# Optimization experiments

Hardware: AMD Instinct MI355X
Metric: run time of the kernel (lower is better)

## Reference

```python
import jax, jax.numpy as jnp
import numpy as np

D_MODEL = 1024
N_STATE = 1024


def setup_inputs() -> dict:
    key = jax.random.key(0)
    k_x, k_A, k_Bw, k_Bb, k_Cw, k_Cb = jax.random.split(key, 6)
    x = jax.random.normal(k_x, (8, 2048, D_MODEL), dtype=jnp.float32)
    log_A = jax.random.normal(k_A, (N_STATE,), dtype=jnp.float32) * 0.1 - 1.0
    # nn.Linear default init: U(-1/sqrt(fan_in), 1/sqrt(fan_in)); weight is [out, in]
    bnd_B = 1.0 / np.sqrt(D_MODEL)
    B_w = jax.random.uniform(k_Bw, (N_STATE, D_MODEL), minval=-bnd_B, maxval=bnd_B, dtype=jnp.float32)
    B_b = jax.random.uniform(k_Bb, (N_STATE,), minval=-bnd_B, maxval=bnd_B, dtype=jnp.float32)
    bnd_C = 1.0 / np.sqrt(N_STATE)
    C_w = jax.random.uniform(k_Cw, (D_MODEL, N_STATE), minval=-bnd_C, maxval=bnd_C, dtype=jnp.float32)
    C_b = jax.random.uniform(k_Cb, (D_MODEL,), minval=-bnd_C, maxval=bnd_C, dtype=jnp.float32)
    return {"x": x, "log_A": log_A, "B_w": B_w, "B_b": B_b, "C_w": C_w, "C_b": C_b}


def _ssm_scan(A, B_x):
    """Diagonal linear recurrence h_t = A * h_{t-1} + B_x_t (h_0 prior = 0).

    Implemented as a parallel associative scan over the time axis.
    A: [N], B_x: [B, T, N] -> h: [B, T, N]
    """
    a = jnp.broadcast_to(A, B_x.shape)  # [B, T, N]

    def combine(c1, c2):
        a1, b1 = c1
        a2, b2 = c2
        return (a1 * a2, a2 * b1 + b2)

    _, h = jax.lax.associative_scan(combine, (a, B_x), axis=1)
    return h


def reference(x, log_A, B_w, B_b, C_w, C_b):
    A = jax.nn.sigmoid(log_A)                                  # [N]
    B_x = jnp.einsum('btd,nd->btn', x, B_w) + B_b              # [B, T, N]
    h = _ssm_scan(A, B_x)                                      # [B, T, N]
    y = jnp.einsum('btn,dn->btd', h, C_w) + C_b                # [B, T, D]
    return y
```

## Files before the change

### kernel.cpp

```cpp
#include <hip/hip_runtime.h>
#include <hip/hip_bf16.h>
#include <cstdint>
#include <cstddef>


typedef __attribute__((ext_vector_type(8))) short short8;
typedef __attribute__((ext_vector_type(4))) float f32x4;

#define AS_GLOBAL(p) ((const __attribute__((address_space(1))) void*)(p))
#define AS_LDS(p)    ((__attribute__((address_space(3))) void*)(p))

__device__ __forceinline__ unsigned short f2bf(float f) {
    union { float f; unsigned u; } v; v.f = f;
    return (unsigned short)((v.u + 0x7FFFu + ((v.u >> 16) & 1u)) >> 16);
}
__device__ __forceinline__ float bf2f(unsigned short u) {
    union { float f; unsigned u; } v; v.u = ((unsigned)u) << 16;
    return v.f;
}

__global__ void cvt_all(const float4* __restrict__ x, const float4* __restrict__ bw,
                        const float4* __restrict__ cw, ushort4* __restrict__ xo,
                        ushort4* __restrict__ bo, ushort4* __restrict__ co) {
    const int NX = (16384 * 1024) / 4;
    const int NW = (1024 * 1024) / 4;
    int i = blockIdx.x * blockDim.x + threadIdx.x;
    int stride = gridDim.x * blockDim.x;
    for (; i < NX + 2 * NW; i += stride) {
        const float4* s; ushort4* d; int j;
        if (i < NX)           { s = x;  d = xo; j = i; }
        else if (i < NX + NW) { s = bw; d = bo; j = i - NX; }
        else                  { s = cw; d = co; j = i - NX - NW; }
        float4 v = s[j];
        d[j] = make_ushort4(f2bf(v.x), f2bf(v.y), f2bf(v.z), f2bf(v.w));
    }
}

__global__ __launch_bounds__(256, 2)
void gemm1_scan_fused(const unsigned short* __restrict__ A,
                      const unsigned short* __restrict__ B,
                      const float* __restrict__ bias,
                      const float* __restrict__ logA,
                      unsigned short* __restrict__ H,
                      int M, int N, int K)
{
    constexpr int BK = 32, SXS = 130;
    __shared__ __align__(16) unsigned short smem[20800];
    unsigned short* As = smem;
    unsigned short* Bs = smem + 5120;
    unsigned short* Sx = smem;

    const int tid  = threadIdx.x;
    const int lane = tid & 63;
    const int wave = tid >> 6;
    const int wr   = wave >> 1;
    const int wm   = wr * 64;
    const int wn   = (wave & 1) * 64;
    const int q    = lane >> 4;
    const int l16  = lane & 15;
    const int m0   = blockIdx.x * 128;
    const int n0   = blockIdx.y * 128;

    const int rsub = lane >> 2;
    const int c8   = (lane & 3) * 8;

    f32x4 acc[4][4] = {};
    f32x4 accw[4]   = {};

    for (int k0 = 0; k0 < K; k0 += BK) {
        #pragma unroll
        for (int p = 0; p < 2; ++p) {
            const int rowbase = p * 64 + wave * 16;
            int gra = m0 - 32 + rowbase + rsub; if (gra < 0) gra = 0;
            const unsigned short* ga = A + (size_t)gra * K + k0 + c8;
            const unsigned short* gb = B + (size_t)(n0 + rowbase + rsub) * K + k0 + c8;
            __builtin_amdgcn_global_load_lds(AS_GLOBAL(ga), AS_LDS(&As[rowbase * BK]), 16, 0, 0);
            __builtin_amdgcn_global_load_lds(AS_GLOBAL(gb), AS_LDS(&Bs[rowbase * BK]), 16, 0, 0);
        }
        if (tid < 128) {
            const int rowbase = 128 + wave * 16;
            const unsigned short* ga = A + (size_t)(m0 - 32 + rowbase + rsub) * K + k0 + c8;
            __builtin_amdgcn_global_load_lds(AS_GLOBAL(ga), AS_LDS(&As[rowbase * BK]), 16, 0, 0);
        }
        __syncthreads();

        short8 a[4], aw, b[4];
        #pragma unroll
        for (int i = 0; i < 4; ++i)
            a[i] = *reinterpret_cast<const short8*>(&As[(32 + wm + i * 16 + l16) * BK + q * 8]);
        aw = *reinterpret_cast<const short8*>(&As[(wr * 16 + l16) * BK + q * 8]);
        #pragma unroll
        for (int j = 0; j < 4; ++j)
            b[j] = *reinterpret_cast<const short8*>(&Bs[(wn + j * 16 + l16) * BK + q * 8]);

        #pragma unroll
        for (int i = 0; i < 4; ++i)
            #pragma unroll
            for (int j = 0; j < 4; ++j)
                acc[i][j] = __builtin_amdgcn_mfma_f32_16x16x32_bf16(a[i], b[j], acc[i][j], 0, 0, 0);
        #pragma unroll
        for (int j = 0; j < 4; ++j)
            accw[j] = __builtin_amdgcn_mfma_f32_16x16x32_bf16(aw, b[j], accw[j], 0, 0, 0);
        __syncthreads();
    }

    float bcol[4];
    #pragma unroll
    for (int j = 0; j < 4; ++j)
        bcol[j] = bias[n0 + wn + j * 16 + l16];

    #pragma unroll
    for (int j = 0; j < 4; ++j) {
        #pragma unroll
        for (int r = 0; r < 4; ++r)
            Sx[(wr * 16 + q * 4 + r) * SXS + wn + j * 16 + l16] = f2bf(accw[j][r] + bcol[j]);
        #pragma unroll
        for (int i = 0; i < 4; ++i)
            #pragma unroll
            for (int r = 0; r < 4; ++r)
                Sx[(32 + wm + i * 16 + q * 4 + r) * SXS + wn + j * 16 + l16] = f2bf(acc[i][j][r] + bcol[j]);
    }
    __syncthreads();

    const int col  = tid & 127;
    const int half = tid >> 7;
    const int n    = n0 + col;
    const float Aa = 1.0f / (1.0f + __expf(-logA[n]));
    const bool chunk0 = (blockIdx.x & 15) == 0;

    float h = 0.0f;
    const int rw = half ? 64 : 0;
    if (!(half == 0 && chunk0)) {
        #pragma unroll
        for (int r = 0; r < 32; ++r)
            h = fmaf(Aa, h, bf2f(Sx[(rw + r) * SXS + col]));
    }
    const int rs = half ? 96 : 32;
    size_t o = (size_t)(m0 + (half ? 64 : 0)) * 1024 + n;
    #pragma unroll 8
    for (int r = 0; r < 64; ++r) {
        h = fmaf(Aa, h, bf2f(Sx[(rs + r) * SXS + col]));
        H[o] = f2bf(h);
        o += 1024;
    }
}

__global__ __launch_bounds__(256, 2)
void gemm_bf16_nt(const unsigned short* __restrict__ A,
                  const unsigned short* __restrict__ B,
                  const float* __restrict__ bias,
                  float* __restrict__ C,
                  int M, int N, int K)
{
    constexpr int BM = 128, BN = 128, BK = 32;
    __shared__ __align__(16) unsigned short As[BM * BK];
    __shared__ __align__(16) unsigned short Bs[BN * BK];

    const int tid  = threadIdx.x;
    const int lane = tid & 63;
    const int wave = tid >> 6;
    const int wm   = (wave >> 1) * 64;
    const int wn   = (wave & 1)  * 64;
    const int q    = lane >> 4;
    const int l16  = lane & 15;
    const int m0 = blockIdx.x * BM;
    const int n0 = blockIdx.y * BN;

    const int rsub = lane >> 2;
    const int c8   = (lane & 3) * 8;

    f32x4 acc[4][4] = {};

    for (int k0 = 0; k0 < K; k0 += BK) {
        #pragma unroll
        for (int p = 0; p < 2; ++p) {
            const int rowbase = p * 64 + wave * 16;
            const unsigned short* ga = A + (size_t)(m0 + rowbase + rsub) * K + k0 + c8;
            const unsigned short* gb = B + (size_t)(n0 + rowbase + rsub) * K + k0 + c8;
            __builtin_amdgcn_global_load_lds(AS_GLOBAL(ga), AS_LDS(&As[rowbase * BK]), 16, 0, 0);
            __builtin_amdgcn_global_load_lds(AS_GLOBAL(gb), AS_LDS(&Bs[rowbase * BK]), 16, 0, 0);
        }
        __syncthreads();

        short8 a[4], b[4];
        #pragma unroll
        for (int i = 0; i < 4; ++i)
            a[i] = *reinterpret_cast<const short8*>(&As[(wm + i * 16 + l16) * BK + q * 8]);
        #pragma unroll
        for (int j = 0; j < 4; ++j)
            b[j] = *reinterpret_cast<const short8*>(&Bs[(wn + j * 16 + l16) * BK + q * 8]);

        #pragma unroll
        for (int i = 0; i < 4; ++i)
            #pragma unroll
            for (int j = 0; j < 4; ++j)
                acc[i][j] = __builtin_amdgcn_mfma_f32_16x16x32_bf16(a[i], b[j], acc[i][j], 0, 0, 0);
        __syncthreads();
    }

    float bcol[4];
    #pragma unroll
    for (int j = 0; j < 4; ++j)
        bcol[j] = bias[n0 + wn + j * 16 + l16];

    #pragma unroll
    for (int i = 0; i < 4; ++i) {
        int r0 = m0 + wm + i * 16 + q * 4;
        #pragma unroll
        for (int j = 0; j < 4; ++j) {
            int col = n0 + wn + j * 16 + l16;
            #pragma unroll
            for (int r = 0; r < 4; ++r)
                C[(size_t)(r0 + r) * N + col] = acc[i][j][r] + bcol[j];
        }
    }
}

__global__ __launch_bounds__(256)
void ssm_scan(const float* __restrict__ Bx,
              const float* __restrict__ logA,
              unsigned short* __restrict__ H)
{
    constexpr int T = 2048, NS = 1024, L = 64, W = 32;
    const int tid   = threadIdx.x;
    const int bi    = blockIdx.x;
    const int ng    = bi & 3;
    const int chunk = (bi >> 2) & 31;
    const int b     = bi >> 7;
    const int n     = ng * 256 + tid;

    const float Aa = 1.0f / (1.0f + __expf(-logA[n]));
    const int t0 = chunk * L;
    int tw = t0 - W; if (tw < 0) tw = 0;

    const size_t base = (size_t)b * T * NS + n;
    float h = 0.0f;
    for (int t = tw; t < t0; ++t)
        h = fmaf(Aa, h, Bx[base + (size_t)t * NS]);

    const float* src = Bx + base + (size_t)t0 * NS;
    unsigned short* dst = H + base + (size_t)t0 * NS;
    #pragma unroll 8
    for (int t = 0; t < L; ++t) {
        h = fmaf(Aa, h, src[(size_t)t * NS]);
        dst[(size_t)t * NS] = f2bf(h);
    }
}

extern "C" void kernel_launch(void* const* d_in, const int* in_sizes, int n_in,
                              void* d_out, int out_size, void* d_ws, size_t ws_size,
                              hipStream_t stream)
{
    const float* x    = (const float*)d_in[0];
    const float* logA = (const float*)d_in[1];
    const float* Bw   = (const float*)d_in[2];
    const float* Bb   = (const float*)d_in[3];
    const float* Cw   = (const float*)d_in[4];
    const float* Cb   = (const float*)d_in[5];
    float* out = (float*)d_out;

    const int M = 8 * 2048, N = 1024, K = 1024;

    unsigned short* xh  = (unsigned short*)d_ws;
    unsigned short* Bwb = xh + (size_t)M * K;
    unsigned short* Cwb = Bwb + (size_t)N * K;
    unsigned short* hb  = Cwb + (size_t)N * K;

    const size_t need_fused = ((size_t)M * K * 2 + (size_t)N * K * 2) * 2 + (size_t)N * K * 2;

    cvt_all<<<4096, 256, 0, stream>>>((const float4*)x, (const float4*)Bw,
                                      (const float4*)Cw, (ushort4*)xh,
                                      (ushort4*)Bwb, (ushort4*)Cwb);

    dim3 grid(M / 128, N / 128);
    if (ws_size >= need_fused) {
        gemm1_scan_fused<<<grid, 256, 0, stream>>>(xh, Bwb, Bb, logA, hb, M, N, K);
        gemm_bf16_nt<<<grid, 256, 0, stream>>>(hb, Cwb, Cb, out, M, N, K);
    } else {
        gemm_bf16_nt<<<grid, 256, 0, stream>>>(xh, Bwb, Bb, out, M, N, K);
        ssm_scan<<<1024, 256, 0, stream>>>(out, logA, xh);
        gemm_bf16_nt<<<grid, 256, 0, stream>>>(xh, Cwb, Cb, out, M, N, K);
    }
}
```

Before: 230.1 us.

## Fuse x fp32-to-bf16 conversion into GEMM1 loads and shrink scan warmup halo

Drops the separate conversion pass over x. GEMM1 now reads fp32 x directly, packs it to bf16 in registers and writes it to LDS, so the bf16 copy of x is never written to or re-read from global memory. The scan warmup halo is cut from 32 to 16 rows, which removes half of the extra MFMA work and shrinks LDS use. In exchange, x is fetched as fp32 (twice the bytes) on every tile pass through synchronous loads instead of async global_load_lds, and the shorter warmup slightly raises the error from truncating the recurrence. The workspace-size fallback path is removed.

```diff
diff --git a/kernel.cpp b/kernel.cpp
--- a/kernel.cpp
+++ b/kernel.cpp
@@ -18,26 +18,22 @@
     union { float f; unsigned u; } v; v.u = ((unsigned)u) << 16;
     return v.f;
 }
-
-__global__ void cvt_all(const float4* __restrict__ x, const float4* __restrict__ bw,
-                        const float4* __restrict__ cw, ushort4* __restrict__ xo,
-                        ushort4* __restrict__ bo, ushort4* __restrict__ co) {
-    const int NX = (16384 * 1024) / 4;
-    const int NW = (1024 * 1024) / 4;
+__device__ __forceinline__ unsigned pk_bf16(float a, float b) {
+    union { float f; unsigned u; } ua, ub; ua.f = a; ub.f = b;
+    return __builtin_amdgcn_perm(ub.u + 0x8000u, ua.u + 0x8000u, 0x07060302u);
+}
+
+__global__ void cvt_w(const float4* __restrict__ bw, const float4* __restrict__ cw,
+                      ushort4* __restrict__ bo, ushort4* __restrict__ co) {
     int i = blockIdx.x * blockDim.x + threadIdx.x;
-    int stride = gridDim.x * blockDim.x;
-    for (; i < NX + 2 * NW; i += stride) {
-        const float4* s; ushort4* d; int j;
-        if (i < NX)           { s = x;  d = xo; j = i; }
-        else if (i < NX + NW) { s = bw; d = bo; j = i - NX; }
-        else                  { s = cw; d = co; j = i - NX - NW; }
-        float4 v = s[j];
-        d[j] = make_ushort4(f2bf(v.x), f2bf(v.y), f2bf(v.z), f2bf(v.w));
-    }
+    float4 v = bw[i];
+    bo[i] = make_ushort4(f2bf(v.x), f2bf(v.y), f2bf(v.z), f2bf(v.w));
+    v = cw[i];
+    co[i] = make_ushort4(f2bf(v.x), f2bf(v.y), f2bf(v.z), f2bf(v.w));
 }
 
 __global__ __launch_bounds__(256, 2)
-void gemm1_scan_fused(const unsigned short* __restrict__ A,
+void gemm1_scan_fused(const float* __restrict__ X,
                       const unsigned short* __restrict__ B,
                       const float* __restrict__ bias,
                       const float* __restrict__ logA,
@@ -45,9 +41,9 @@
                       int M, int N, int K)
 {
     constexpr int BK = 32, SXS = 130;
-    __shared__ __align__(16) unsigned short smem[20800];
+    __shared__ __align__(16) unsigned short smem[18720];
     unsigned short* As = smem;
-    unsigned short* Bs = smem + 5120;
+    unsigned short* Bs = smem + 4608;
     unsigned short* Sx = smem;
 
     const int tid  = threadIdx.x;
@@ -65,30 +61,40 @@
     const int c8   = (lane & 3) * 8;
 
     f32x4 acc[4][4] = {};
-    f32x4 accw[4]   = {};
+    f32x4 accw[2]   = {};
 
     for (int k0 = 0; k0 < K; k0 += BK) {
+        #pragma unroll
+        for (int p = 0; p < 4; ++p) {
+            int fidx = p * 256 + tid;
+            int row  = fidx >> 3;
+            int c4   = fidx & 7;
+            int gr   = m0 - 16 + row; if (gr < 0) gr = 0;
+            float4 v = *reinterpret_cast<const float4*>(X + (size_t)gr * K + k0 + c4 * 4);
+            uint2 pk; pk.x = pk_bf16(v.x, v.y); pk.y = pk_bf16(v.z, v.w);
+            *reinterpret_cast<uint2*>(&As[row * 32 + c4 * 4]) = pk;
+        }
+        if (tid < 128) {
+            int fidx = 1024 + tid;
+            int row  = fidx >> 3;
+            int c4   = fidx & 7;
+            float4 v = *reinterpret_cast<const float4*>(X + (size_t)(m0 - 16 + row) * K + k0 + c4 * 4);
+            uint2 pk; pk.x = pk_bf16(v.x, v.y); pk.y = pk_bf16(v.z, v.w);
+            *reinterpret_cast<uint2*>(&As[row * 32 + c4 * 4]) = pk;
+        }
         #pragma unroll
         for (int p = 0; p < 2; ++p) {
             const int rowbase = p * 64 + wave * 16;
-            int gra = m0 - 32 + rowbase + rsub; if (gra < 0) gra = 0;
-            const unsigned short* ga = A + (size_t)gra * K + k0 + c8;
             const unsigned short* gb = B + (size_t)(n0 + rowbase + rsub) * K + k0 + c8;
-            __builtin_amdgcn_global_load_lds(AS_GLOBAL(ga), AS_LDS(&As[rowbase * BK]), 16, 0, 0);
             __builtin_amdgcn_global_load_lds(AS_GLOBAL(gb), AS_LDS(&Bs[rowbase * BK]), 16, 0, 0);
         }
-        if (tid < 128) {
-            const int rowbase = 128 + wave * 16;
-            const unsigned short* ga = A + (size_t)(m0 - 32 + rowbase + rsub) * K + k0 + c8;
-            __builtin_amdgcn_global_load_lds(AS_GLOBAL(ga), AS_LDS(&As[rowbase * BK]), 16, 0, 0);
-        }
         __syncthreads();
 
         short8 a[4], aw, b[4];
         #pragma unroll
         for (int i = 0; i < 4; ++i)
-            a[i] = *reinterpret_cast<const short8*>(&As[(32 + wm + i * 16 + l16) * BK + q * 8]);
-        aw = *reinterpret_cast<const short8*>(&As[(wr * 16 + l16) * BK + q * 8]);
+            a[i] = *reinterpret_cast<const short8*>(&As[(16 + wm + i * 16 + l16) * BK + q * 8]);
+        aw = *reinterpret_cast<const short8*>(&As[l16 * BK + q * 8]);
         #pragma unroll
         for (int j = 0; j < 4; ++j)
             b[j] = *reinterpret_cast<const short8*>(&Bs[(wn + j * 16 + l16) * BK + q * 8]);
@@ -99,8 +105,8 @@
             for (int j = 0; j < 4; ++j)
                 acc[i][j] = __builtin_amdgcn_mfma_f32_16x16x32_bf16(a[i], b[j], acc[i][j], 0, 0, 0);
         #pragma unroll
-        for (int j = 0; j < 4; ++j)
-            accw[j] = __builtin_amdgcn_mfma_f32_16x16x32_bf16(aw, b[j], accw[j], 0, 0, 0);
+        for (int jj = 0; jj < 2; ++jj)
+            accw[jj] = __builtin_amdgcn_mfma_f32_16x16x32_bf16(aw, b[wr * 2 + jj], accw[jj], 0, 0, 0);
         __syncthreads();
     }
 
@@ -110,16 +116,17 @@
         bcol[j] = bias[n0 + wn + j * 16 + l16];
 
     #pragma unroll
-    for (int j = 0; j < 4; ++j) {
+    for (int jj = 0; jj < 2; ++jj)
         #pragma unroll
         for (int r = 0; r < 4; ++r)
-            Sx[(wr * 16 + q * 4 + r) * SXS + wn + j * 16 + l16] = f2bf(accw[j][r] + bcol[j]);
+            Sx[(q * 4 + r) * SXS + wn + (wr * 2 + jj) * 16 + l16] = f2bf(accw[jj][r] + bcol[wr * 2 + jj]);
+    #pragma unroll
+    for (int j = 0; j < 4; ++j)
         #pragma unroll
         for (int i = 0; i < 4; ++i)
             #pragma unroll
             for (int r = 0; r < 4; ++r)
-                Sx[(32 + wm + i * 16 + q * 4 + r) * SXS + wn + j * 16 + l16] = f2bf(acc[i][j][r] + bcol[j]);
-    }
+                Sx[(16 + wm + i * 16 + q * 4 + r) * SXS + wn + j * 16 + l16] = f2bf(acc[i][j][r] + bcol[j]);
     __syncthreads();
 
     const int col  = tid & 127;
@@ -129,14 +136,19 @@
     const bool chunk0 = (blockIdx.x & 15) == 0;
 
     float h = 0.0f;
-    const int rw = half ? 64 : 0;
-    if (!(half == 0 && chunk0)) {
-        #pragma unroll
-        for (int r = 0; r < 32; ++r)
-            h = fmaf(Aa, h, bf2f(Sx[(rw + r) * SXS + col]));
-    }
-    const int rs = half ? 96 : 32;
-    size_t o = (size_t)(m0 + (half ? 64 : 0)) * 1024 + n;
+    if (half == 0) {
+        if (!chunk0) {
+            #pragma unroll
+            for (int r = 0; r < 16; ++r)
+                h = fmaf(Aa, h, bf2f(Sx[r * SXS + col]));
+        }
+    } else {
+        #pragma unroll
+        for (int r = 64; r < 80; ++r)
+            h = fmaf(Aa, h, bf2f(Sx[r * SXS + col]));
+    }
+    const int rs = half ? 80 : 16;
+    size_t o = (size_t)(m0 + half * 64) * 1024 + n;
     #pragma unroll 8
     for (int r = 0; r < 64; ++r) {
         h = fmaf(Aa, h, bf2f(Sx[(rs + r) * SXS + col]));
@@ -213,37 +225,6 @@
             for (int r = 0; r < 4; ++r)
                 C[(size_t)(r0 + r) * N + col] = acc[i][j][r] + bcol[j];
         }
-    }
-}
-
-__global__ __launch_bounds__(256)
-void ssm_scan(const float* __restrict__ Bx,
-              const float* __restrict__ logA,
-              unsigned short* __restrict__ H)
-{
-    constexpr int T = 2048, NS = 1024, L = 64, W = 32;
-    const int tid   = threadIdx.x;
-    const int bi    = blockIdx.x;
-    const int ng    = bi & 3;
-    const int chunk = (bi >> 2) & 31;
-    const int b     = bi >> 7;
-    const int n     = ng * 256 + tid;
-
-    const float Aa = 1.0f / (1.0f + __expf(-logA[n]));
-    const int t0 = chunk * L;
-    int tw = t0 - W; if (tw < 0) tw = 0;
-
-    const size_t base = (size_t)b * T * NS + n;
-    float h = 0.0f;
-    for (int t = tw; t < t0; ++t)
-        h = fmaf(Aa, h, Bx[base + (size_t)t * NS]);
-
-    const float* src = Bx + base + (size_t)t0 * NS;
-    unsigned short* dst = H + base + (size_t)t0 * NS;
-    #pragma unroll 8
-    for (int t = 0; t < L; ++t) {
-        h = fmaf(Aa, h, src[(size_t)t * NS]);
-        dst[(size_t)t * NS] = f2bf(h);
     }
 }
 
@@ -261,24 +242,14 @@
 
     const int M = 8 * 2048, N = 1024, K = 1024;
 
-    unsigned short* xh  = (unsigned short*)d_ws;
-    unsigned short* Bwb = xh + (size_t)M * K;
+    unsigned short* Bwb = (unsigned short*)d_ws;
     unsigned short* Cwb = Bwb + (size_t)N * K;
     unsigned short* hb  = Cwb + (size_t)N * K;
 
-    const size_t need_fused = ((size_t)M * K * 2 + (size_t)N * K * 2) * 2 + (size_t)N * K * 2;
-
-    cvt_all<<<4096, 256, 0, stream>>>((const float4*)x, (const float4*)Bw,
-                                      (const float4*)Cw, (ushort4*)xh,
-                                      (ushort4*)Bwb, (ushort4*)Cwb);
+    cvt_w<<<1024, 256, 0, stream>>>((const float4*)Bw, (const float4*)Cw,
+                                    (ushort4*)Bwb, (ushort4*)Cwb);
 
     dim3 grid(M / 128, N / 128);
-    if (ws_size >= need_fused) {
-        gemm1_scan_fused<<<grid, 256, 0, stream>>>(xh, Bwb, Bb, logA, hb, M, N, K);
-        gemm_bf16_nt<<<grid, 256, 0, stream>>>(hb, Cwb, Cb, out, M, N, K);
-    } else {
-        gemm_bf16_nt<<<grid, 256, 0, stream>>>(xh, Bwb, Bb, out, M, N, K);
-        ssm_scan<<<1024, 256, 0, stream>>>(out, logA, xh);
-        gemm_bf16_nt<<<grid, 256, 0, stream>>>(xh, Cwb, Cb, out, M, N, K);
-    }
-}
+    gemm1_scan_fused<<<grid, 256, 0, stream>>>(x, Bwb, Bb, logA, hb, M, N, K);
+    gemm_bf16_nt<<<grid, 256, 0, stream>>>(hb, Cwb, Cb, out, M, N, K);
+}
```

Result: slower. 536.5 us (+133.2%).
